# Optimization experiments

Hardware: AMD Instinct MI355X
Metric: run time of the kernel (lower is better)

Reference implementation:

```python
import jax, jax.numpy as jnp
import numpy as np

B, S, D = 8, 4096, 1024
EPS = 1e-8  # torch F.cosine_similarity default eps


def setup_inputs() -> dict:
    key = jax.random.key(0)
    kx, kwq, kbq, kwk, kbk = jax.random.split(key, 5)
    bound = 1.0 / np.sqrt(D)  # torch nn.Linear default init
    return {
        "x": jax.random.normal(kx, (B, S, D), dtype=jnp.float32),
        "Wq": jax.random.uniform(kwq, (D, D), jnp.float32, -bound, bound),
        "bq": jax.random.uniform(kbq, (D,), jnp.float32, -bound, bound),
        "Wk": jax.random.uniform(kwk, (D, D), jnp.float32, -bound, bound),
        "bk": jax.random.uniform(kbk, (D,), jnp.float32, -bound, bound),
    }


def reference(x, Wq, bq, Wk, bk):
    # ---- RoutingModule ----
    q = jnp.einsum("bsd,ed->bse", x, Wq) + bq                      # [B,S,D]
    x_roll = jnp.roll(x, shift=1, axis=1)                           # roll along seq
    k = jnp.einsum("bsd,ed->bse", x_roll, Wk) + bk                  # [B,S,D]
    qn = q / jnp.maximum(jnp.linalg.norm(q, axis=-1, keepdims=True), EPS)
    kn = k / jnp.maximum(jnp.linalg.norm(k, axis=-1, keepdims=True), EPS)
    cosine_sim = jnp.sum(qn * kn, axis=-1)                          # [B,S]
    p = 0.5 * (1.0 - cosine_sim)
    p = p.at[:, 0].set(1.0)
    b = (p >= 0.5).astype(x.dtype)                                  # [B,S]

    # ---- ragged compaction into padded buffer ----
    # Stable argsort moves selected positions to the front, preserving order.
    order = jnp.argsort(1.0 - b, axis=1)                            # [B,S] int
    gathered = jnp.take_along_axis(x, order[:, :, None], axis=1)    # [B,S,D]
    counts = jnp.sum(b, axis=1).astype(jnp.int32)                   # [B]
    valid = jnp.arange(S)[None, :] < counts[:, None]                # [B,S]
    # Padded to S (static max possible length) for jit-compatibility; torch
    # trims to the batch max, but all rows beyond each count are zeros here too.
    selected_padded = jnp.where(valid[:, :, None], gathered, 0.0)   # [B,S,D]
    return selected_padded, p, b
```

## Files before the change

kernel.cpp:

```cpp
#include <hip/hip_runtime.h>
#include <stdint.h>

#define Bb 8
#define Ss 4096
#define Dd 1024
#define Mm (Bb*Ss)
#define Kk 1024

typedef _Float16 half8 __attribute__((ext_vector_type(8)));
typedef _Float16 half4v __attribute__((ext_vector_type(4)));
typedef float f32x4 __attribute__((ext_vector_type(4)));

#define LO_SCALE 2048.0f
#define INV_LO_SCALE (1.0f/2048.0f)

__device__ __forceinline__ void gld_lds16(const void* g, void* l) {
  __builtin_amdgcn_global_load_lds(
      (const __attribute__((address_space(1))) unsigned int*)g,
      (__attribute__((address_space(3))) unsigned int*)l, 16, 0, 0);
}

__global__ void split_w3(const float* __restrict__ Gp, const float* __restrict__ Wq,
                         const float* __restrict__ Wk,
                         _Float16* __restrict__ Gh, _Float16* __restrict__ Gl,
                         _Float16* __restrict__ Wh) {
  const int which = blockIdx.y;
  const int i = blockIdx.x * 256 + threadIdx.x;
  float4 v;
  if (which == 0) {
    float4 v0 = ((const float4*)Gp)[i];
    float4 v1 = ((const float4*)(Gp + (size_t)Dd * Dd))[i];
    float4 v2 = ((const float4*)(Gp + (size_t)2 * Dd * Dd))[i];
    float4 v3 = ((const float4*)(Gp + (size_t)3 * Dd * Dd))[i];
    v.x = (v0.x + v1.x) + (v2.x + v3.x);
    v.y = (v0.y + v1.y) + (v2.y + v3.y);
    v.z = (v0.z + v1.z) + (v2.z + v3.z);
    v.w = (v0.w + v1.w) + (v2.w + v3.w);
  } else {
    const float* src = (which == 1) ? Wq : Wk;
    v = ((const float4*)src)[i];
  }
  _Float16 h0 = (_Float16)v.x, h1 = (_Float16)v.y, h2 = (_Float16)v.z, h3 = (_Float16)v.w;
  if (which == 0) {
    _Float16 l0 = (_Float16)((v.x - (float)h0) * LO_SCALE);
    _Float16 l1 = (_Float16)((v.y - (float)h1) * LO_SCALE);
    _Float16 l2 = (_Float16)((v.z - (float)h2) * LO_SCALE);
    _Float16 l3 = (_Float16)((v.w - (float)h3) * LO_SCALE);
    ((half4v*)Gh)[i] = (half4v){h0, h1, h2, h3};
    ((half4v*)Gl)[i] = (half4v){l0, l1, l2, l3};
  } else {
    _Float16* hi = (which == 1) ? Wh : Wh + (size_t)Dd * Dd;
    ((half4v*)hi)[i] = (half4v){h0, h1, h2, h3};
  }
}

__global__ void split_x(const float* __restrict__ X, const float* __restrict__ up,
                        const float* __restrict__ vp,
                        _Float16* __restrict__ Xh, _Float16* __restrict__ Xl,
                        float* __restrict__ a_u, float* __restrict__ a_v) {
  const int s = blockIdx.x * 4 + (threadIdx.x >> 6);
  const int lane = threadIdx.x & 63;
  float au = 0.f, av = 0.f;
#pragma unroll
  for (int c = 0; c < 4; ++c) {
    const int e = c * 256 + lane * 4;
    float4 xv = *(const float4*)&X[(size_t)s * Dd + e];
    float4 uv = {0.f, 0.f, 0.f, 0.f}, vv = {0.f, 0.f, 0.f, 0.f};
#pragma unroll
    for (int z = 0; z < 4; ++z) {
      float4 a = *(const float4*)&up[(size_t)z * Dd + e];
      float4 b = *(const float4*)&vp[(size_t)z * Dd + e];
      uv.x += a.x; uv.y += a.y; uv.z += a.z; uv.w += a.w;
      vv.x += b.x; vv.y += b.y; vv.z += b.z; vv.w += b.w;
    }
    _Float16 h0 = (_Float16)xv.x, h1 = (_Float16)xv.y, h2 = (_Float16)xv.z, h3 = (_Float16)xv.w;
    _Float16 l0 = (_Float16)((xv.x - (float)h0) * LO_SCALE);
    _Float16 l1 = (_Float16)((xv.y - (float)h1) * LO_SCALE);
    _Float16 l2 = (_Float16)((xv.z - (float)h2) * LO_SCALE);
    _Float16 l3 = (_Float16)((xv.w - (float)h3) * LO_SCALE);
    *(half4v*)&Xh[(size_t)s * Dd + e] = (half4v){h0, h1, h2, h3};
    *(half4v*)&Xl[(size_t)s * Dd + e] = (half4v){l0, l1, l2, l3};
    au += uv.x * xv.x + uv.y * xv.y + uv.z * xv.z + uv.w * xv.w;
    av += vv.x * xv.x + vv.y * xv.y + vv.z * xv.z + vv.w * xv.w;
  }
#pragma unroll
  for (int off = 32; off > 0; off >>= 1) {
    au += __shfl_xor(au, off);
    av += __shfl_xor(av, off);
  }
  if (lane == 0) { a_u[s] = au; a_v[s] = av; }
}

__global__ __launch_bounds__(256)
void gemm_g_part(const float* __restrict__ Wq, const float* __restrict__ Wk,
                 float* __restrict__ Gp) {
  __shared__ float As[16][64];
  __shared__ float Bs[16][64];
  const int t = threadIdx.x;
  const int m0 = blockIdx.y * 64, n0 = blockIdx.x * 64;
  const int kbase = blockIdx.z * 256;
  float acc[4][4];
#pragma unroll
  for (int a = 0; a < 4; ++a)
#pragma unroll
    for (int b = 0; b < 4; ++b) acc[a][b] = 0.f;
  for (int kc = 0; kc < 16; ++kc) {
    const int k0 = kbase + kc * 16;
#pragma unroll
    for (int l = 0; l < 4; ++l) {
      const int idx = l * 256 + t;
      const int kk = idx >> 6, mm = idx & 63;
      As[kk][mm] = Wq[(size_t)(k0 + kk) * Dd + m0 + mm];
      Bs[kk][mm] = Wk[(size_t)(k0 + kk) * Dd + n0 + mm];
    }
    __syncthreads();
    const int tm = (t & 15) * 4, tn = (t >> 4) * 4;
#pragma unroll
    for (int k = 0; k < 16; ++k) {
      float4 a4 = *(const float4*)&As[k][tm];
      float4 b4 = *(const float4*)&Bs[k][tn];
      const float aa[4] = {a4.x, a4.y, a4.z, a4.w};
      const float bb[4] = {b4.x, b4.y, b4.z, b4.w};
#pragma unroll
      for (int a = 0; a < 4; ++a)
#pragma unroll
        for (int b = 0; b < 4; ++b) acc[a][b] += aa[a] * bb[b];
    }
    __syncthreads();
  }
  float* dst = Gp + (size_t)blockIdx.z * Dd * Dd;
  const int tm = (t & 15) * 4, tn = (t >> 4) * 4;
#pragma unroll
  for (int a = 0; a < 4; ++a)
#pragma unroll
    for (int b = 0; b < 4; ++b)
      dst[(size_t)(m0 + tm + a) * Dd + n0 + tn + b] = acc[a][b];
}

__global__ void uvc_part(const float* __restrict__ Wq, const float* __restrict__ Wk,
                         const float* __restrict__ bq, const float* __restrict__ bk,
                         float* __restrict__ up, float* __restrict__ vp,
                         float* __restrict__ c) {
  const int bx = blockIdx.x;
  if (bx == 32) {
    const int lane = threadIdx.x;
    if (lane >= 64) return;
    float a = 0.f;
#pragma unroll
    for (int i = 0; i < 16; ++i) a += bq[lane * 16 + i] * bk[lane * 16 + i];
#pragma unroll
    for (int off = 32; off > 0; off >>= 1) a += __shfl_xor(a, off);
    if (lane == 0) *c = a;
    return;
  }
  const int echunk = bx & 3;
  const int which = (bx >> 2) & 1;
  const int dchunk = bx >> 3;
  const int d = dchunk * 256 + threadIdx.x;
  const float* W = which ? Wq : Wk;
  const float* bb = which ? bk : bq;
  float acc = 0.f;
  const int e0 = echunk * 256;
#pragma unroll 4
  for (int e = e0; e < e0 + 256; ++e) acc += bb[e] * W[(size_t)e * Dd + d];
  float* dst = which ? vp : up;
  dst[(size_t)echunk * Dd + d] = acc;
}

__global__ __launch_bounds__(256, 2)
void gemm_dot(const _Float16* __restrict__ Ah, const _Float16* __restrict__ Al,
              const _Float16* __restrict__ Gh, const _Float16* __restrict__ Gl,
              const float* __restrict__ X, float* __restrict__ pd) {
  __shared__ __align__(16) _Float16 smem[4 * 128 * 64];
  _Float16* AsH = smem;
  _Float16* AsL = smem + 8192;
  _Float16* BsH = smem + 16384;
  _Float16* BsL = smem + 24576;
  const int tid = threadIdx.x;
  const int wave = tid >> 6, lane = tid & 63;
  const int m0 = blockIdx.y * 128, n0 = blockIdx.x * 128;
  const int wm = (wave >> 1) * 64, wn = (wave & 1) * 64;
  const int fr = lane & 15, g = lane >> 4;
  const int srow8 = lane >> 3, s8 = lane & 7;

  f32x4 accH[4][4], accX[4][4];
#pragma unroll
  for (int i = 0; i < 4; ++i)
#pragma unroll
    for (int j = 0; j < 4; ++j) {
      accH[i][j] = (f32x4){0.f, 0.f, 0.f, 0.f};
      accX[i][j] = (f32x4){0.f, 0.f, 0.f, 0.f};
    }

  for (int kt = 0; kt < Kk / 64; ++kt) {
    const int k0 = kt * 64;
#pragma unroll
    for (int it = 0; it < 4; ++it) {
      const int R = wave * 32 + it * 8 + srow8;
      const int gcol = k0 + ((s8 ^ (R & 7)) * 8);
      const int ldsoff = (wave * 32 + it * 8) * 64;
      const size_t ga = (size_t)(m0 + R) * Kk + gcol;
      const size_t gb = (size_t)(n0 + R) * Kk + gcol;
      gld_lds16(Ah + ga, &AsH[ldsoff]);
      gld_lds16(Al + ga, &AsL[ldsoff]);
      gld_lds16(Gh + gb, &BsH[ldsoff]);
      gld_lds16(Gl + gb, &BsL[ldsoff]);
    }
    __syncthreads();
#pragma unroll
    for (int kk = 0; kk < 2; ++kk) {
      const int gg = kk * 4 + g;
      half8 bh[4], bl[4];
#pragma unroll
      for (int j = 0; j < 4; ++j) {
        const int R = wn + 16 * j + fr;
        const int sl = (gg ^ (R & 7)) * 8;
        bh[j] = *(const half8*)&BsH[R * 64 + sl];
        bl[j] = *(const half8*)&BsL[R * 64 + sl];
      }
#pragma unroll
      for (int i = 0; i < 4; ++i) {
        const int R = wm + 16 * i + fr;
        const int sl = (gg ^ (R & 7)) * 8;
        half8 ah = *(const half8*)&AsH[R * 64 + sl];
        half8 al = *(const half8*)&AsL[R * 64 + sl];
#pragma unroll
        for (int j = 0; j < 4; ++j) {
          accH[i][j] = __builtin_amdgcn_mfma_f32_16x16x32_f16(ah, bh[j], accH[i][j], 0, 0, 0);
          accX[i][j] = __builtin_amdgcn_mfma_f32_16x16x32_f16(ah, bl[j], accX[i][j], 0, 0, 0);
          accX[i][j] = __builtin_amdgcn_mfma_f32_16x16x32_f16(al, bh[j], accX[i][j], 0, 0, 0);
        }
      }
    }
    __syncthreads();
  }
  const int quad = lane >> 4;
  const int slot = blockIdx.x * 2 + (wave & 1);
#pragma unroll
  for (int i = 0; i < 4; ++i) {
#pragma unroll
    for (int r = 0; r < 4; ++r) {
      const int s = m0 + wm + 16 * i + quad * 4 + r;
      const int t = s + 1;
      float dsum = 0.f;
      if ((t & (Ss - 1)) != 0) {
        const float* xrow = X + (size_t)t * Dd + n0 + wn;
#pragma unroll
        for (int j = 0; j < 4; ++j) {
          float yv = accH[i][j][r] + accX[i][j][r] * INV_LO_SCALE;
          dsum += yv * xrow[16 * j + fr];
        }
      }
      dsum += __shfl_xor(dsum, 1);
      dsum += __shfl_xor(dsum, 2);
      dsum += __shfl_xor(dsum, 4);
      dsum += __shfl_xor(dsum, 8);
      if (fr == 0 && ((t & (Ss - 1)) != 0))
        pd[(size_t)slot * Mm + t] = dsum;
    }
  }
}

__global__ __launch_bounds__(256, 3)
void gemm_norm(const _Float16* __restrict__ Ah, const _Float16* __restrict__ Wh,
               const float* __restrict__ bq, const float* __restrict__ bk,
               float* __restrict__ pn) {
  __shared__ __align__(16) _Float16 smem[2 * 128 * 64];
  _Float16* NA = smem;
  _Float16* NB = smem + 8192;
  const int tid = threadIdx.x;
  const int wave = tid >> 6, lane = tid & 63;
  const int m0 = blockIdx.y * 128, n0 = blockIdx.x * 128;
  const int wm = (wave >> 1) * 64, wn = (wave & 1) * 64;
  const int fr = lane & 15, g = lane >> 4;
  const int srow8 = lane >> 3, s8 = lane & 7;

  f32x4 acc[4][4];
#pragma unroll
  for (int i = 0; i < 4; ++i)
#pragma unroll
    for (int j = 0; j < 4; ++j) acc[i][j] = (f32x4){0.f, 0.f, 0.f, 0.f};

  for (int kt = 0; kt < Kk / 64; ++kt) {
    const int k0 = kt * 64;
#pragma unroll
    for (int it = 0; it < 4; ++it) {
      const int R = wave * 32 + it * 8 + srow8;
      const int gcol = k0 + ((s8 ^ (R & 7)) * 8);
      const int ldsoff = (wave * 32 + it * 8) * 64;
      gld_lds16(Ah + (size_t)(m0 + R) * Kk + gcol, &NA[ldsoff]);
      gld_lds16(Wh + (size_t)(n0 + R) * Kk + gcol, &NB[ldsoff]);
    }
    __syncthreads();
#pragma unroll
    for (int kk = 0; kk < 2; ++kk) {
      const int gg = kk * 4 + g;
      half8 bh[4];
#pragma unroll
      for (int j = 0; j < 4; ++j) {
        const int R = wn + 16 * j + fr;
        bh[j] = *(const half8*)&NB[R * 64 + (gg ^ (R & 7)) * 8];
      }
#pragma unroll
      for (int i = 0; i < 4; ++i) {
        const int R = wm + 16 * i + fr;
        half8 ah = *(const half8*)&NA[R * 64 + (gg ^ (R & 7)) * 8];
#pragma unroll
        for (int j = 0; j < 4; ++j)
          acc[i][j] = __builtin_amdgcn_mfma_f32_16x16x32_f16(ah, bh[j], acc[i][j], 0, 0, 0);
      }
    }
    __syncthreads();
  }
  const int quad = lane >> 4;
  float bias_j[4];
#pragma unroll
  for (int j = 0; j < 4; ++j) {
    const int n = n0 + wn + 16 * j + fr;
    bias_j[j] = (n < Dd) ? bq[n] : bk[n - Dd];
  }
  const int slot = blockIdx.x * 2 + (wave & 1);
#pragma unroll
  for (int i = 0; i < 4; ++i) {
#pragma unroll
    for (int r = 0; r < 4; ++r) {
      float vsum = 0.f;
#pragma unroll
      for (int j = 0; j < 4; ++j) {
        float q = acc[i][j][r] + bias_j[j];
        vsum += q * q;
      }
      vsum += __shfl_xor(vsum, 1);
      vsum += __shfl_xor(vsum, 2);
      vsum += __shfl_xor(vsum, 4);
      vsum += __shfl_xor(vsum, 8);
      if (fr == 0)
        pn[(size_t)slot * Mm + (m0 + wm + 16 * i + quad * 4 + r)] = vsum;
    }
  }
}

__global__ void cos_final(const float* __restrict__ pd, const float* __restrict__ pn,
                          const float* __restrict__ a_u, const float* __restrict__ a_v,
                          const float* __restrict__ cptr,
                          float* __restrict__ p_out, float* __restrict__ b_out) {
  const int s = blockIdx.x * 256 + threadIdx.x;
  if ((s & (Ss - 1)) == 0) { p_out[s] = 1.0f; b_out[s] = 1.0f; return; }
  float dot = a_u[s - 1] + a_v[s] + *cptr;
#pragma unroll
  for (int sl = 0; sl < 16; ++sl) dot += pd[(size_t)sl * Mm + s];
  float nq = 0.f, nk = 0.f;
#pragma unroll
  for (int sl = 0; sl < 16; ++sl) nq += pn[(size_t)sl * Mm + s];
#pragma unroll
  for (int sl = 16; sl < 32; ++sl) nk += pn[(size_t)sl * Mm + (s - 1)];
  float denom = fmaxf(sqrtf(nq), 1e-8f) * fmaxf(sqrtf(nk), 1e-8f);
  float cs = dot / denom;
  float p = 0.5f * (1.0f - cs);
  p_out[s] = p;
  b_out[s] = (p >= 0.5f) ? 1.0f : 0.0f;
}

__global__ __launch_bounds__(1024)
void scan_flags(const float* __restrict__ b_out,
                int* __restrict__ sel, int* __restrict__ counts) {
  const int b = blockIdx.x;
  const int tid = threadIdx.x;
  const int lane = tid & 63;
  const int w = tid >> 6;
  __shared__ int wtot[16];
  float fv[4];
#pragma unroll
  for (int c = 0; c < 4; ++c) fv[c] = b_out[b * Ss + c * 1024 + tid];
  int running = 0;
#pragma unroll
  for (int c = 0; c < 4; ++c) {
    const bool f = fv[c] != 0.0f;
    unsigned long long m = __ballot(f);
    int pre = __popcll(m & ((1ull << lane) - 1ull));
    if (lane == 0) wtot[w] = __popcll(m);
    __syncthreads();
    int woff = 0, tot = 0;
#pragma unroll
    for (int ww = 0; ww < 16; ++ww) {
      int t = wtot[ww];
      if (ww < w) woff += t;
      tot += t;
    }
    if (f) sel[b * Ss + running + woff + pre] = c * 1024 + tid;
    running += tot;
    __syncthreads();
  }
  if (tid == 0) counts[b] = running;
}

__global__ void write_out(const float* __restrict__ x, const int* __restrict__ sel,
                          const int* __restrict__ counts, float* __restrict__ out) {
  const int blk = blockIdx.x;
  const int b = blk >> 12;
  const int r = blk & (Ss - 1);
  const int tid = threadIdx.x;
  float4 v = {0.f, 0.f, 0.f, 0.f};
  if (r < counts[b]) {
    const int src = sel[b * Ss + r];
    v = *(const float4*)&x[((size_t)b * Ss + src) * Dd + tid * 4];
  }
  *(float4*)&out[(size_t)blk * Dd + tid * 4] = v;
}

extern "C" void kernel_launch(void* const* d_in, const int* in_sizes, int n_in,
                              void* d_out, int out_size, void* d_ws, size_t ws_size,
                              hipStream_t stream) {
  const float* x  = (const float*)d_in[0];
  const float* Wq = (const float*)d_in[1];
  const float* bq = (const float*)d_in[2];
  const float* Wk = (const float*)d_in[3];
  const float* bk = (const float*)d_in[4];
  float* out = (float*)d_out;

  uint8_t* w = (uint8_t*)d_ws;
  _Float16* Xh = (_Float16*)w;   w += (size_t)Mm * Kk * 2;
  _Float16* Xl = (_Float16*)w;   w += (size_t)Mm * Kk * 2;
  float*    Gp = (float*)w;      w += (size_t)4 * Dd * Dd * 4;
  _Float16* Gh = (_Float16*)w;   w += (size_t)Dd * Dd * 2;
  _Float16* Gl = (_Float16*)w;   w += (size_t)Dd * Dd * 2;
  _Float16* Wh = (_Float16*)w;   w += (size_t)2 * Dd * Dd * 2;
  float* pd = (float*)w;         w += (size_t)16 * Mm * 4;
  float* pn = (float*)w;         w += (size_t)32 * Mm * 4;
  float* a_u = (float*)w;        w += (size_t)Mm * 4;
  float* a_v = (float*)w;        w += (size_t)Mm * 4;
  float* up  = (float*)w;        w += (size_t)4 * Dd * 4;
  float* vp  = (float*)w;        w += (size_t)4 * Dd * 4;
  float* cpt = (float*)w;        w += 64;
  int*   sel = (int*)w;          w += (size_t)Mm * 4;
  int*   counts = (int*)w;       w += 64;

  float* p_out = out + (size_t)Mm * Dd;
  float* b_out = p_out + Mm;

  gemm_g_part<<<dim3(16, 16, 4), 256, 0, stream>>>(Wq, Wk, Gp);
  uvc_part<<<33, 256, 0, stream>>>(Wq, Wk, bq, bk, up, vp, cpt);
  split_x<<<Mm / 4, 256, 0, stream>>>(x, up, vp, Xh, Xl, a_u, a_v);
  split_w3<<<dim3((Dd * Dd / 4) / 256, 3), 256, 0, stream>>>(Gp, Wq, Wk, Gh, Gl, Wh);
  gemm_norm<<<dim3(2 * Dd / 128, Mm / 128), 256, 0, stream>>>(Xh, Wh, bq, bk, pn);
  gemm_dot<<<dim3(Dd / 128, Mm / 128), 256, 0, stream>>>(Xh, Xl, Gh, Gl, x, pd);
  cos_final<<<Mm / 256, 256, 0, stream>>>(pd, pn, a_u, a_v, cpt, p_out, b_out);
  scan_flags<<<Bb, 1024, 0, stream>>>(b_out, sel, counts);
  write_out<<<Mm, 256, 0, stream>>>(x, sel, counts, out);
}
```

Baseline: 708.6 us.

## Interleave hi/lo halves and triple-buffer both GEMMs with larger tiles

The hi and lo fp16 splits of x and G are interleaved into one row-major buffer, so one async load brings both halves. Both GEMM kernels move to 512 threads with 256x128 tiles, a three-slot LDS ring with explicit vmcnt waits, a tile swizzle for locality, and raised wave priority around the MFMA blocks. Per-wave partial row sums are reduced in LDS before storing, which halves the partial-slot buffers that cos_final reads. The aim is to hide global-load latency and cut barriers and partial traffic, at the cost of more LDS use and register pressure.

```diff
diff --git a/kernel.cpp b/kernel.cpp
--- a/kernel.cpp
+++ b/kernel.cpp
@@ -22,8 +22,7 @@
 
 __global__ void split_w3(const float* __restrict__ Gp, const float* __restrict__ Wq,
                          const float* __restrict__ Wk,
-                         _Float16* __restrict__ Gh, _Float16* __restrict__ Gl,
-                         _Float16* __restrict__ Wh) {
+                         _Float16* __restrict__ G2, _Float16* __restrict__ Wh) {
   const int which = blockIdx.y;
   const int i = blockIdx.x * 256 + threadIdx.x;
   float4 v;
@@ -46,8 +45,9 @@
     _Float16 l1 = (_Float16)((v.y - (float)h1) * LO_SCALE);
     _Float16 l2 = (_Float16)((v.z - (float)h2) * LO_SCALE);
     _Float16 l3 = (_Float16)((v.w - (float)h3) * LO_SCALE);
-    ((half4v*)Gh)[i] = (half4v){h0, h1, h2, h3};
-    ((half4v*)Gl)[i] = (half4v){l0, l1, l2, l3};
+    const int n = i >> 8, c = i & 255;
+    ((half4v*)G2)[(size_t)n * 512 + c]       = (half4v){h0, h1, h2, h3};
+    ((half4v*)G2)[(size_t)n * 512 + 256 + c] = (half4v){l0, l1, l2, l3};
   } else {
     _Float16* hi = (which == 1) ? Wh : Wh + (size_t)Dd * Dd;
     ((half4v*)hi)[i] = (half4v){h0, h1, h2, h3};
@@ -56,7 +56,7 @@
 
 __global__ void split_x(const float* __restrict__ X, const float* __restrict__ up,
                         const float* __restrict__ vp,
-                        _Float16* __restrict__ Xh, _Float16* __restrict__ Xl,
+                        _Float16* __restrict__ X2,
                         float* __restrict__ a_u, float* __restrict__ a_v) {
   const int s = blockIdx.x * 4 + (threadIdx.x >> 6);
   const int lane = threadIdx.x & 63;
@@ -78,8 +78,8 @@
     _Float16 l1 = (_Float16)((xv.y - (float)h1) * LO_SCALE);
     _Float16 l2 = (_Float16)((xv.z - (float)h2) * LO_SCALE);
     _Float16 l3 = (_Float16)((xv.w - (float)h3) * LO_SCALE);
-    *(half4v*)&Xh[(size_t)s * Dd + e] = (half4v){h0, h1, h2, h3};
-    *(half4v*)&Xl[(size_t)s * Dd + e] = (half4v){l0, l1, l2, l3};
+    *(half4v*)&X2[(size_t)s * 2048 + e]        = (half4v){h0, h1, h2, h3};
+    *(half4v*)&X2[(size_t)s * 2048 + 1024 + e] = (half4v){l0, l1, l2, l3};
     au += uv.x * xv.x + uv.y * xv.y + uv.z * xv.z + uv.w * xv.w;
     av += vv.x * xv.x + vv.y * xv.y + vv.z * xv.z + vv.w * xv.w;
   }
@@ -167,86 +167,126 @@
   dst[(size_t)echunk * Dd + d] = acc;
 }
 
-__global__ __launch_bounds__(256, 2)
-void gemm_dot(const _Float16* __restrict__ Ah, const _Float16* __restrict__ Al,
-              const _Float16* __restrict__ Gh, const _Float16* __restrict__ Gl,
+
+__global__ __launch_bounds__(512, 2)
+void gemm_dot(const _Float16* __restrict__ X2, const _Float16* __restrict__ G2,
               const float* __restrict__ X, float* __restrict__ pd) {
-  __shared__ __align__(16) _Float16 smem[4 * 128 * 64];
-  _Float16* AsH = smem;
-  _Float16* AsL = smem + 8192;
-  _Float16* BsH = smem + 16384;
-  _Float16* BsL = smem + 24576;
+  __shared__ __align__(16) _Float16 smem[3 * 24576];
   const int tid = threadIdx.x;
   const int wave = tid >> 6, lane = tid & 63;
-  const int m0 = blockIdx.y * 128, n0 = blockIdx.x * 128;
-  const int wm = (wave >> 1) * 64, wn = (wave & 1) * 64;
-  const int fr = lane & 15, g = lane >> 4;
-  const int srow8 = lane >> 3, s8 = lane & 7;
-
-  f32x4 accH[4][4], accX[4][4];
-#pragma unroll
-  for (int i = 0; i < 4; ++i)
-#pragma unroll
-    for (int j = 0; j < 4; ++j) {
+  const int lin = blockIdx.y * 8 + blockIdx.x;
+  const int logical = (lin & 7) * 128 + (lin >> 3);
+  const int n0 = (logical & 7) * 128;
+  const int m0 = (logical >> 3) * 256;
+  const int wm = (wave >> 2) * 128;
+  const int wn = (wave & 3) * 32;
+  const int fr = lane & 15, g4 = lane >> 4;
+  const int sr = lane >> 3, sc = lane & 7;
+
+  size_t aoff[4];
+  size_t boff[2];
+#pragma unroll
+  for (int st = 0; st < 4; ++st) {
+    const int R = st * 64 + wave * 8 + sr;
+    const int u = sc ^ (R & 7);
+    aoff[st] = (size_t)(m0 + R) * 2048 + ((u & 3) << 3) + ((size_t)(u >> 2) << 10);
+  }
+#pragma unroll
+  for (int st = 0; st < 2; ++st) {
+    const int R = st * 64 + wave * 8 + sr;
+    const int u = sc ^ (R & 7);
+    boff[st] = (size_t)(n0 + R) * 2048 + ((u & 3) << 3) + ((size_t)(u >> 2) << 10);
+  }
+  int aro[2][8], bro[2][2];
+#pragma unroll
+  for (int i = 0; i < 8; ++i) {
+    const int Ra = wm + i * 16 + fr;
+    aro[0][i] = Ra * 64 + ((g4 ^ (Ra & 7)) << 3);
+    aro[1][i] = Ra * 64 + (((4 | g4) ^ (Ra & 7)) << 3);
+  }
+#pragma unroll
+  for (int j = 0; j < 2; ++j) {
+    const int Rb = wn + j * 16 + fr;
+    bro[0][j] = Rb * 64 + ((g4 ^ (Rb & 7)) << 3);
+    bro[1][j] = Rb * 64 + (((4 | g4) ^ (Rb & 7)) << 3);
+  }
+
+  f32x4 accH[8][2], accX[8][2];
+#pragma unroll
+  for (int i = 0; i < 8; ++i)
+#pragma unroll
+    for (int j = 0; j < 2; ++j) {
       accH[i][j] = (f32x4){0.f, 0.f, 0.f, 0.f};
       accX[i][j] = (f32x4){0.f, 0.f, 0.f, 0.f};
     }
 
-  for (int kt = 0; kt < Kk / 64; ++kt) {
-    const int k0 = kt * 64;
-#pragma unroll
-    for (int it = 0; it < 4; ++it) {
-      const int R = wave * 32 + it * 8 + srow8;
-      const int gcol = k0 + ((s8 ^ (R & 7)) * 8);
-      const int ldsoff = (wave * 32 + it * 8) * 64;
-      const size_t ga = (size_t)(m0 + R) * Kk + gcol;
-      const size_t gb = (size_t)(n0 + R) * Kk + gcol;
-      gld_lds16(Ah + ga, &AsH[ldsoff]);
-      gld_lds16(Al + ga, &AsL[ldsoff]);
-      gld_lds16(Gh + gb, &BsH[ldsoff]);
-      gld_lds16(Gl + gb, &BsL[ldsoff]);
-    }
-    __syncthreads();
-#pragma unroll
-    for (int kk = 0; kk < 2; ++kk) {
-      const int gg = kk * 4 + g;
-      half8 bh[4], bl[4];
-#pragma unroll
-      for (int j = 0; j < 4; ++j) {
-        const int R = wn + 16 * j + fr;
-        const int sl = (gg ^ (R & 7)) * 8;
-        bh[j] = *(const half8*)&BsH[R * 64 + sl];
-        bl[j] = *(const half8*)&BsL[R * 64 + sl];
+#define DOT_STAGE(kt, slot) do {                                      \
+    const size_t kof = (size_t)(kt) * 32;                             \
+    _Float16* sb_ = smem + (slot) * 24576;                            \
+    gld_lds16(X2 + aoff[0] + kof, sb_ + 0 * 4096 + wave * 512);       \
+    gld_lds16(X2 + aoff[1] + kof, sb_ + 1 * 4096 + wave * 512);       \
+    gld_lds16(X2 + aoff[2] + kof, sb_ + 2 * 4096 + wave * 512);       \
+    gld_lds16(X2 + aoff[3] + kof, sb_ + 3 * 4096 + wave * 512);       \
+    gld_lds16(G2 + boff[0] + kof, sb_ + 16384 + 0 * 4096 + wave * 512); \
+    gld_lds16(G2 + boff[1] + kof, sb_ + 16384 + 1 * 4096 + wave * 512); \
+  } while (0)
+
+  DOT_STAGE(0, 0);
+  DOT_STAGE(1, 1);
+  int slot = 0;
+  for (int kt = 0; kt < 32; ++kt) {
+    if (kt < 31) asm volatile("s_waitcnt vmcnt(6)" ::: "memory");
+    else         asm volatile("s_waitcnt vmcnt(0)" ::: "memory");
+    __builtin_amdgcn_s_barrier();
+    asm volatile("" ::: "memory");
+    if (kt + 2 < 32) {
+      int s2 = slot + 2; if (s2 >= 3) s2 -= 3;
+      DOT_STAGE(kt + 2, s2);
+    }
+    const _Float16* A  = smem + slot * 24576;
+    const _Float16* Bm = A + 16384;
+    half8 bh[2], bl[2];
+#pragma unroll
+    for (int j = 0; j < 2; ++j) {
+      bh[j] = *(const half8*)&Bm[bro[0][j]];
+      bl[j] = *(const half8*)&Bm[bro[1][j]];
+    }
+#pragma unroll
+    for (int ph = 0; ph < 4; ++ph) {
+      const int i0 = ph * 2;
+      half8 ah0 = *(const half8*)&A[aro[0][i0]];
+      half8 al0 = *(const half8*)&A[aro[1][i0]];
+      half8 ah1 = *(const half8*)&A[aro[0][i0 + 1]];
+      half8 al1 = *(const half8*)&A[aro[1][i0 + 1]];
+      __builtin_amdgcn_s_setprio(1);
+#pragma unroll
+      for (int j = 0; j < 2; ++j) {
+        accH[i0][j]     = __builtin_amdgcn_mfma_f32_16x16x32_f16(ah0, bh[j], accH[i0][j], 0, 0, 0);
+        accX[i0][j]     = __builtin_amdgcn_mfma_f32_16x16x32_f16(ah0, bl[j], accX[i0][j], 0, 0, 0);
+        accX[i0][j]     = __builtin_amdgcn_mfma_f32_16x16x32_f16(al0, bh[j], accX[i0][j], 0, 0, 0);
+        accH[i0 + 1][j] = __builtin_amdgcn_mfma_f32_16x16x32_f16(ah1, bh[j], accH[i0 + 1][j], 0, 0, 0);
+        accX[i0 + 1][j] = __builtin_amdgcn_mfma_f32_16x16x32_f16(ah1, bl[j], accX[i0 + 1][j], 0, 0, 0);
+        accX[i0 + 1][j] = __builtin_amdgcn_mfma_f32_16x16x32_f16(al1, bh[j], accX[i0 + 1][j], 0, 0, 0);
       }
-#pragma unroll
-      for (int i = 0; i < 4; ++i) {
-        const int R = wm + 16 * i + fr;
-        const int sl = (gg ^ (R & 7)) * 8;
-        half8 ah = *(const half8*)&AsH[R * 64 + sl];
-        half8 al = *(const half8*)&AsL[R * 64 + sl];
-#pragma unroll
-        for (int j = 0; j < 4; ++j) {
-          accH[i][j] = __builtin_amdgcn_mfma_f32_16x16x32_f16(ah, bh[j], accH[i][j], 0, 0, 0);
-          accX[i][j] = __builtin_amdgcn_mfma_f32_16x16x32_f16(ah, bl[j], accX[i][j], 0, 0, 0);
-          accX[i][j] = __builtin_amdgcn_mfma_f32_16x16x32_f16(al, bh[j], accX[i][j], 0, 0, 0);
-        }
-      }
-    }
-    __syncthreads();
-  }
-  const int quad = lane >> 4;
-  const int slot = blockIdx.x * 2 + (wave & 1);
-#pragma unroll
-  for (int i = 0; i < 4; ++i) {
+      __builtin_amdgcn_s_setprio(0);
+    }
+    __builtin_amdgcn_sched_barrier(0);
+    slot = (slot == 2) ? 0 : slot + 1;
+  }
+
+  float* scratch = (float*)smem;
+  const int quad = g4;
+#pragma unroll
+  for (int i = 0; i < 8; ++i) {
 #pragma unroll
     for (int r = 0; r < 4; ++r) {
-      const int s = m0 + wm + 16 * i + quad * 4 + r;
-      const int t = s + 1;
+      const int row = wm + 16 * i + quad * 4 + r;
+      const int t = m0 + row + 1;
       float dsum = 0.f;
       if ((t & (Ss - 1)) != 0) {
         const float* xrow = X + (size_t)t * Dd + n0 + wn;
 #pragma unroll
-        for (int j = 0; j < 4; ++j) {
+        for (int j = 0; j < 2; ++j) {
           float yv = accH[i][j][r] + accX[i][j][r] * INV_LO_SCALE;
           dsum += yv * xrow[16 * j + fr];
         }
@@ -255,78 +295,138 @@
       dsum += __shfl_xor(dsum, 2);
       dsum += __shfl_xor(dsum, 4);
       dsum += __shfl_xor(dsum, 8);
-      if (fr == 0 && ((t & (Ss - 1)) != 0))
-        pd[(size_t)slot * Mm + t] = dsum;
-    }
-  }
-}
-
-__global__ __launch_bounds__(256, 3)
-void gemm_norm(const _Float16* __restrict__ Ah, const _Float16* __restrict__ Wh,
+      if (fr == 0) scratch[row * 4 + (wave & 3)] = dsum;
+    }
+  }
+  __syncthreads();
+  if (tid < 256) {
+    const int t = m0 + tid + 1;
+    if ((t & (Ss - 1)) != 0) {
+      float v = scratch[tid * 4] + scratch[tid * 4 + 1] +
+                scratch[tid * 4 + 2] + scratch[tid * 4 + 3];
+      pd[(size_t)(logical & 7) * Mm + t] = v;
+    }
+  }
+}
+
+__global__ __launch_bounds__(512, 2)
+void gemm_norm(const _Float16* __restrict__ X2, const _Float16* __restrict__ Wh,
                const float* __restrict__ bq, const float* __restrict__ bk,
                float* __restrict__ pn) {
-  __shared__ __align__(16) _Float16 smem[2 * 128 * 64];
-  _Float16* NA = smem;
-  _Float16* NB = smem + 8192;
+  __shared__ __align__(16) _Float16 smem[3 * 24576];
   const int tid = threadIdx.x;
   const int wave = tid >> 6, lane = tid & 63;
-  const int m0 = blockIdx.y * 128, n0 = blockIdx.x * 128;
-  const int wm = (wave >> 1) * 64, wn = (wave & 1) * 64;
-  const int fr = lane & 15, g = lane >> 4;
-  const int srow8 = lane >> 3, s8 = lane & 7;
-
-  f32x4 acc[4][4];
-#pragma unroll
-  for (int i = 0; i < 4; ++i)
-#pragma unroll
-    for (int j = 0; j < 4; ++j) acc[i][j] = (f32x4){0.f, 0.f, 0.f, 0.f};
-
-  for (int kt = 0; kt < Kk / 64; ++kt) {
-    const int k0 = kt * 64;
-#pragma unroll
-    for (int it = 0; it < 4; ++it) {
-      const int R = wave * 32 + it * 8 + srow8;
-      const int gcol = k0 + ((s8 ^ (R & 7)) * 8);
-      const int ldsoff = (wave * 32 + it * 8) * 64;
-      gld_lds16(Ah + (size_t)(m0 + R) * Kk + gcol, &NA[ldsoff]);
-      gld_lds16(Wh + (size_t)(n0 + R) * Kk + gcol, &NB[ldsoff]);
-    }
-    __syncthreads();
-#pragma unroll
-    for (int kk = 0; kk < 2; ++kk) {
-      const int gg = kk * 4 + g;
-      half8 bh[4];
-#pragma unroll
-      for (int j = 0; j < 4; ++j) {
-        const int R = wn + 16 * j + fr;
-        bh[j] = *(const half8*)&NB[R * 64 + (gg ^ (R & 7)) * 8];
+  const int lin = blockIdx.y * 16 + blockIdx.x;
+  const int logical = (lin & 7) * 256 + (lin >> 3);
+  const int n0 = (logical & 15) * 128;
+  const int m0 = (logical >> 4) * 256;
+  const int wm = (wave >> 2) * 128;
+  const int wn = (wave & 3) * 32;
+  const int fr = lane & 15, g4 = lane >> 4;
+  const int sr = lane >> 3, sc = lane & 7;
+
+  size_t aoff[4];
+  size_t boff[2];
+#pragma unroll
+  for (int st = 0; st < 4; ++st) {
+    const int R = st * 64 + wave * 8 + sr;
+    const int u = sc ^ (R & 7);
+    aoff[st] = (size_t)(m0 + R) * 2048 + ((size_t)u << 3);
+  }
+#pragma unroll
+  for (int st = 0; st < 2; ++st) {
+    const int R = st * 64 + wave * 8 + sr;
+    const int u = sc ^ (R & 7);
+    boff[st] = (size_t)(n0 + R) * 1024 + ((size_t)u << 3);
+  }
+  int aro[2][8], bro[2][2];
+#pragma unroll
+  for (int i = 0; i < 8; ++i) {
+    const int Ra = wm + i * 16 + fr;
+    aro[0][i] = Ra * 64 + ((g4 ^ (Ra & 7)) << 3);
+    aro[1][i] = Ra * 64 + (((4 | g4) ^ (Ra & 7)) << 3);
+  }
+#pragma unroll
+  for (int j = 0; j < 2; ++j) {
+    const int Rb = wn + j * 16 + fr;
+    bro[0][j] = Rb * 64 + ((g4 ^ (Rb & 7)) << 3);
+    bro[1][j] = Rb * 64 + (((4 | g4) ^ (Rb & 7)) << 3);
+  }
+
+  f32x4 acc[8][2];
+#pragma unroll
+  for (int i = 0; i < 8; ++i)
+#pragma unroll
+    for (int j = 0; j < 2; ++j) acc[i][j] = (f32x4){0.f, 0.f, 0.f, 0.f};
+
+#define NRM_STAGE(kt, slot) do {                                      \
+    const size_t kof = (size_t)(kt) * 64;                             \
+    _Float16* sb_ = smem + (slot) * 24576;                            \
+    gld_lds16(X2 + aoff[0] + kof, sb_ + 0 * 4096 + wave * 512);       \
+    gld_lds16(X2 + aoff[1] + kof, sb_ + 1 * 4096 + wave * 512);       \
+    gld_lds16(X2 + aoff[2] + kof, sb_ + 2 * 4096 + wave * 512);       \
+    gld_lds16(X2 + aoff[3] + kof, sb_ + 3 * 4096 + wave * 512);       \
+    gld_lds16(Wh + boff[0] + kof, sb_ + 16384 + 0 * 4096 + wave * 512); \
+    gld_lds16(Wh + boff[1] + kof, sb_ + 16384 + 1 * 4096 + wave * 512); \
+  } while (0)
+
+  NRM_STAGE(0, 0);
+  NRM_STAGE(1, 1);
+  int slot = 0;
+  for (int kt = 0; kt < 16; ++kt) {
+    if (kt < 15) asm volatile("s_waitcnt vmcnt(6)" ::: "memory");
+    else         asm volatile("s_waitcnt vmcnt(0)" ::: "memory");
+    __builtin_amdgcn_s_barrier();
+    asm volatile("" ::: "memory");
+    if (kt + 2 < 16) {
+      int s2 = slot + 2; if (s2 >= 3) s2 -= 3;
+      NRM_STAGE(kt + 2, s2);
+    }
+    const _Float16* A  = smem + slot * 24576;
+    const _Float16* Bm = A + 16384;
+    half8 b0[2], b1[2];
+#pragma unroll
+    for (int j = 0; j < 2; ++j) {
+      b0[j] = *(const half8*)&Bm[bro[0][j]];
+      b1[j] = *(const half8*)&Bm[bro[1][j]];
+    }
+#pragma unroll
+    for (int ph = 0; ph < 4; ++ph) {
+      const int i0 = ph * 2;
+      half8 a00 = *(const half8*)&A[aro[0][i0]];
+      half8 a01 = *(const half8*)&A[aro[1][i0]];
+      half8 a10 = *(const half8*)&A[aro[0][i0 + 1]];
+      half8 a11 = *(const half8*)&A[aro[1][i0 + 1]];
+      __builtin_amdgcn_s_setprio(1);
+#pragma unroll
+      for (int j = 0; j < 2; ++j) {
+        acc[i0][j]     = __builtin_amdgcn_mfma_f32_16x16x32_f16(a00, b0[j], acc[i0][j], 0, 0, 0);
+        acc[i0][j]     = __builtin_amdgcn_mfma_f32_16x16x32_f16(a01, b1[j], acc[i0][j], 0, 0, 0);
+        acc[i0 + 1][j] = __builtin_amdgcn_mfma_f32_16x16x32_f16(a10, b0[j], acc[i0 + 1][j], 0, 0, 0);
+        acc[i0 + 1][j] = __builtin_amdgcn_mfma_f32_16x16x32_f16(a11, b1[j], acc[i0 + 1][j], 0, 0, 0);
       }
-#pragma unroll
-      for (int i = 0; i < 4; ++i) {
-        const int R = wm + 16 * i + fr;
-        half8 ah = *(const half8*)&NA[R * 64 + (gg ^ (R & 7)) * 8];
-#pragma unroll
-        for (int j = 0; j < 4; ++j)
-          acc[i][j] = __builtin_amdgcn_mfma_f32_16x16x32_f16(ah, bh[j], acc[i][j], 0, 0, 0);
-      }
-    }
-    __syncthreads();
-  }
-  const int quad = lane >> 4;
-  float bias_j[4];
-#pragma unroll
-  for (int j = 0; j < 4; ++j) {
+      __builtin_amdgcn_s_setprio(0);
+    }
+    __builtin_amdgcn_sched_barrier(0);
+    slot = (slot == 2) ? 0 : slot + 1;
+  }
+
+  float bias_j[2];
+#pragma unroll
+  for (int j = 0; j < 2; ++j) {
     const int n = n0 + wn + 16 * j + fr;
     bias_j[j] = (n < Dd) ? bq[n] : bk[n - Dd];
   }
-  const int slot = blockIdx.x * 2 + (wave & 1);
-#pragma unroll
-  for (int i = 0; i < 4; ++i) {
+  float* scratch = (float*)smem;
+  const int quad = g4;
+#pragma unroll
+  for (int i = 0; i < 8; ++i) {
 #pragma unroll
     for (int r = 0; r < 4; ++r) {
+      const int row = wm + 16 * i + quad * 4 + r;
       float vsum = 0.f;
 #pragma unroll
-      for (int j = 0; j < 4; ++j) {
+      for (int j = 0; j < 2; ++j) {
         float q = acc[i][j][r] + bias_j[j];
         vsum += q * q;
       }
@@ -334,9 +434,14 @@
       vsum += __shfl_xor(vsum, 2);
       vsum += __shfl_xor(vsum, 4);
       vsum += __shfl_xor(vsum, 8);
-      if (fr == 0)
-        pn[(size_t)slot * Mm + (m0 + wm + 16 * i + quad * 4 + r)] = vsum;
-    }
+      if (fr == 0) scratch[row * 4 + (wave & 3)] = vsum;
+    }
+  }
+  __syncthreads();
+  if (tid < 256) {
+    float v = scratch[tid * 4] + scratch[tid * 4 + 1] +
+              scratch[tid * 4 + 2] + scratch[tid * 4 + 3];
+    pn[(size_t)(logical & 15) * Mm + (m0 + tid)] = v;
   }
 }
 
@@ -348,12 +453,12 @@
   if ((s & (Ss - 1)) == 0) { p_out[s] = 1.0f; b_out[s] = 1.0f; return; }
   float dot = a_u[s - 1] + a_v[s] + *cptr;
 #pragma unroll
-  for (int sl = 0; sl < 16; ++sl) dot += pd[(size_t)sl * Mm + s];
+  for (int sl = 0; sl < 8; ++sl) dot += pd[(size_t)sl * Mm + s];
   float nq = 0.f, nk = 0.f;
 #pragma unroll
-  for (int sl = 0; sl < 16; ++sl) nq += pn[(size_t)sl * Mm + s];
-#pragma unroll
-  for (int sl = 16; sl < 32; ++sl) nk += pn[(size_t)sl * Mm + (s - 1)];
+  for (int sl = 0; sl < 8; ++sl) nq += pn[(size_t)sl * Mm + s];
+#pragma unroll
+  for (int sl = 8; sl < 16; ++sl) nk += pn[(size_t)sl * Mm + (s - 1)];
   float denom = fmaxf(sqrtf(nq), 1e-8f) * fmaxf(sqrtf(nk), 1e-8f);
   float cs = dot / denom;
   float p = 0.5f * (1.0f - cs);
@@ -419,31 +524,29 @@
   float* out = (float*)d_out;
 
   uint8_t* w = (uint8_t*)d_ws;
-  _Float16* Xh = (_Float16*)w;   w += (size_t)Mm * Kk * 2;
-  _Float16* Xl = (_Float16*)w;   w += (size_t)Mm * Kk * 2;
-  float*    Gp = (float*)w;      w += (size_t)4 * Dd * Dd * 4;
-  _Float16* Gh = (_Float16*)w;   w += (size_t)Dd * Dd * 2;
-  _Float16* Gl = (_Float16*)w;   w += (size_t)Dd * Dd * 2;
-  _Float16* Wh = (_Float16*)w;   w += (size_t)2 * Dd * Dd * 2;
-  float* pd = (float*)w;         w += (size_t)16 * Mm * 4;
-  float* pn = (float*)w;         w += (size_t)32 * Mm * 4;
-  float* a_u = (float*)w;        w += (size_t)Mm * 4;
-  float* a_v = (float*)w;        w += (size_t)Mm * 4;
-  float* up  = (float*)w;        w += (size_t)4 * Dd * 4;
-  float* vp  = (float*)w;        w += (size_t)4 * Dd * 4;
-  float* cpt = (float*)w;        w += 64;
-  int*   sel = (int*)w;          w += (size_t)Mm * 4;
-  int*   counts = (int*)w;       w += 64;
+  _Float16* X2 = (_Float16*)w; w += (size_t)Mm * 2048 * 2;
+  float*    Gp = (float*)w;    w += (size_t)4 * Dd * Dd * 4;
+  _Float16* G2 = (_Float16*)w; w += (size_t)Dd * 2048 * 2;
+  _Float16* Wh = (_Float16*)w; w += (size_t)2 * Dd * Dd * 2;
+  float* pd = (float*)w;       w += (size_t)8 * Mm * 4;
+  float* pn = (float*)w;       w += (size_t)16 * Mm * 4;
+  float* a_u = (float*)w;      w += (size_t)Mm * 4;
+  float* a_v = (float*)w;      w += (size_t)Mm * 4;
+  float* up  = (float*)w;      w += (size_t)4 * Dd * 4;
+  float* vp  = (float*)w;      w += (size_t)4 * Dd * 4;
+  float* cpt = (float*)w;      w += 64;
+  int*   sel = (int*)w;        w += (size_t)Mm * 4;
+  int*   counts = (int*)w;     w += 64;
 
   float* p_out = out + (size_t)Mm * Dd;
   float* b_out = p_out + Mm;
 
   gemm_g_part<<<dim3(16, 16, 4), 256, 0, stream>>>(Wq, Wk, Gp);
   uvc_part<<<33, 256, 0, stream>>>(Wq, Wk, bq, bk, up, vp, cpt);
-  split_x<<<Mm / 4, 256, 0, stream>>>(x, up, vp, Xh, Xl, a_u, a_v);
-  split_w3<<<dim3((Dd * Dd / 4) / 256, 3), 256, 0, stream>>>(Gp, Wq, Wk, Gh, Gl, Wh);
-  gemm_norm<<<dim3(2 * Dd / 128, Mm / 128), 256, 0, stream>>>(Xh, Wh, bq, bk, pn);
-  gemm_dot<<<dim3(Dd / 128, Mm / 128), 256, 0, stream>>>(Xh, Xl, Gh, Gl, x, pd);
+  split_x<<<Mm / 4, 256, 0, stream>>>(x, up, vp, X2, a_u, a_v);
+  split_w3<<<dim3((Dd * Dd / 4) / 256, 3), 256, 0, stream>>>(Gp, Wq, Wk, G2, Wh);
+  gemm_norm<<<dim3(16, Mm / 256), 512, 0, stream>>>(X2, Wh, bq, bk, pn);
+  gemm_dot<<<dim3(8, Mm / 256), 512, 0, stream>>>(X2, G2, x, pd);
   cos_final<<<Mm / 256, 256, 0, stream>>>(pd, pn, a_u, a_v, cpt, p_out, b_out);
   scan_flags<<<Bb, 1024, 0, stream>>>(b_out, sel, counts);
   write_out<<<Mm, 256, 0, stream>>>(x, sel, counts, out);
```

New measurement: 782.1 us. 1.1x slower.

## Interleave hi/lo fp16 splits and read G operand directly from global memory

Applied to the files above, without the earlier changes.

Computes G = Wq^T Wk in one non-split-K kernel that writes hi/lo fp16 halves directly, which removes the partial-sum buffer and the reduction in the split kernel. X and G hi/lo halves are interleaved per row into single buffers. gemm_dot no longer stages the G tile in LDS: B fragments are loaded straight from global or L2, which halves shared memory use and may raise occupancy. The cost is uncoalesced, uncached-in-LDS B reads repeated across waves, and gemm_g now runs with only 256 blocks and a long K loop.

```diff
diff --git a/kernel.cpp b/kernel.cpp
--- a/kernel.cpp
+++ b/kernel.cpp
@@ -20,43 +20,74 @@
       (__attribute__((address_space(3))) unsigned int*)l, 16, 0, 0);
 }
 
-__global__ void split_w3(const float* __restrict__ Gp, const float* __restrict__ Wq,
-                         const float* __restrict__ Wk,
-                         _Float16* __restrict__ Gh, _Float16* __restrict__ Gl,
+#define MFMA16(d, a, b) d = __builtin_amdgcn_mfma_f32_16x16x32_f16(a, b, d, 0, 0, 0)
+
+__global__ __launch_bounds__(256)
+void gemm_g(const float* __restrict__ Wq, const float* __restrict__ Wk,
+            _Float16* __restrict__ G2) {
+  __shared__ float As[16][64];
+  __shared__ float Bs[16][64];
+  const int t = threadIdx.x;
+  const int m0 = blockIdx.y * 64, n0 = blockIdx.x * 64;
+  float acc[4][4];
+#pragma unroll
+  for (int a = 0; a < 4; ++a)
+#pragma unroll
+    for (int b = 0; b < 4; ++b) acc[a][b] = 0.f;
+  for (int kc = 0; kc < 64; ++kc) {
+    const int k0 = kc * 16;
+#pragma unroll
+    for (int l = 0; l < 4; ++l) {
+      const int idx = l * 256 + t;
+      const int kk = idx >> 6, mm = idx & 63;
+      As[kk][mm] = Wq[(size_t)(k0 + kk) * Dd + m0 + mm];
+      Bs[kk][mm] = Wk[(size_t)(k0 + kk) * Dd + n0 + mm];
+    }
+    __syncthreads();
+    const int tm = (t & 15) * 4, tn = (t >> 4) * 4;
+#pragma unroll
+    for (int k = 0; k < 16; ++k) {
+      float4 a4 = *(const float4*)&As[k][tm];
+      float4 b4 = *(const float4*)&Bs[k][tn];
+      const float aa[4] = {a4.x, a4.y, a4.z, a4.w};
+      const float bb[4] = {b4.x, b4.y, b4.z, b4.w};
+#pragma unroll
+      for (int a = 0; a < 4; ++a)
+#pragma unroll
+        for (int b = 0; b < 4; ++b) acc[a][b] += aa[a] * bb[b];
+    }
+    __syncthreads();
+  }
+  const int tm = (t & 15) * 4, tn = (t >> 4) * 4;
+#pragma unroll
+  for (int a = 0; a < 4; ++a) {
+    half4v hv, lv;
+#pragma unroll
+    for (int b = 0; b < 4; ++b) {
+      float v = acc[a][b];
+      _Float16 h = (_Float16)v;
+      hv[b] = h;
+      lv[b] = (_Float16)((v - (float)h) * LO_SCALE);
+    }
+    const size_t row = (size_t)(m0 + tm + a) * 2048;
+    *(half4v*)&G2[row + n0 + tn] = hv;
+    *(half4v*)&G2[row + 1024 + n0 + tn] = lv;
+  }
+}
+
+__global__ void split_w2(const float* __restrict__ Wq, const float* __restrict__ Wk,
                          _Float16* __restrict__ Wh) {
   const int which = blockIdx.y;
   const int i = blockIdx.x * 256 + threadIdx.x;
-  float4 v;
-  if (which == 0) {
-    float4 v0 = ((const float4*)Gp)[i];
-    float4 v1 = ((const float4*)(Gp + (size_t)Dd * Dd))[i];
-    float4 v2 = ((const float4*)(Gp + (size_t)2 * Dd * Dd))[i];
-    float4 v3 = ((const float4*)(Gp + (size_t)3 * Dd * Dd))[i];
-    v.x = (v0.x + v1.x) + (v2.x + v3.x);
-    v.y = (v0.y + v1.y) + (v2.y + v3.y);
-    v.z = (v0.z + v1.z) + (v2.z + v3.z);
-    v.w = (v0.w + v1.w) + (v2.w + v3.w);
-  } else {
-    const float* src = (which == 1) ? Wq : Wk;
-    v = ((const float4*)src)[i];
-  }
-  _Float16 h0 = (_Float16)v.x, h1 = (_Float16)v.y, h2 = (_Float16)v.z, h3 = (_Float16)v.w;
-  if (which == 0) {
-    _Float16 l0 = (_Float16)((v.x - (float)h0) * LO_SCALE);
-    _Float16 l1 = (_Float16)((v.y - (float)h1) * LO_SCALE);
-    _Float16 l2 = (_Float16)((v.z - (float)h2) * LO_SCALE);
-    _Float16 l3 = (_Float16)((v.w - (float)h3) * LO_SCALE);
-    ((half4v*)Gh)[i] = (half4v){h0, h1, h2, h3};
-    ((half4v*)Gl)[i] = (half4v){l0, l1, l2, l3};
-  } else {
-    _Float16* hi = (which == 1) ? Wh : Wh + (size_t)Dd * Dd;
-    ((half4v*)hi)[i] = (half4v){h0, h1, h2, h3};
-  }
+  const float* src = which ? Wk : Wq;
+  float4 v = ((const float4*)src)[i];
+  _Float16* dst = Wh + (size_t)which * Dd * Dd;
+  ((half4v*)dst)[i] = (half4v){(_Float16)v.x, (_Float16)v.y, (_Float16)v.z, (_Float16)v.w};
 }
 
 __global__ void split_x(const float* __restrict__ X, const float* __restrict__ up,
                         const float* __restrict__ vp,
-                        _Float16* __restrict__ Xh, _Float16* __restrict__ Xl,
+                        _Float16* __restrict__ X2,
                         float* __restrict__ a_u, float* __restrict__ a_v) {
   const int s = blockIdx.x * 4 + (threadIdx.x >> 6);
   const int lane = threadIdx.x & 63;
@@ -78,8 +109,8 @@
     _Float16 l1 = (_Float16)((xv.y - (float)h1) * LO_SCALE);
     _Float16 l2 = (_Float16)((xv.z - (float)h2) * LO_SCALE);
     _Float16 l3 = (_Float16)((xv.w - (float)h3) * LO_SCALE);
-    *(half4v*)&Xh[(size_t)s * Dd + e] = (half4v){h0, h1, h2, h3};
-    *(half4v*)&Xl[(size_t)s * Dd + e] = (half4v){l0, l1, l2, l3};
+    *(half4v*)&X2[(size_t)s * 2048 + e]        = (half4v){h0, h1, h2, h3};
+    *(half4v*)&X2[(size_t)s * 2048 + 1024 + e] = (half4v){l0, l1, l2, l3};
     au += uv.x * xv.x + uv.y * xv.y + uv.z * xv.z + uv.w * xv.w;
     av += vv.x * xv.x + vv.y * xv.y + vv.z * xv.z + vv.w * xv.w;
   }
@@ -89,52 +120,6 @@
     av += __shfl_xor(av, off);
   }
   if (lane == 0) { a_u[s] = au; a_v[s] = av; }
-}
-
-__global__ __launch_bounds__(256)
-void gemm_g_part(const float* __restrict__ Wq, const float* __restrict__ Wk,
-                 float* __restrict__ Gp) {
-  __shared__ float As[16][64];
-  __shared__ float Bs[16][64];
-  const int t = threadIdx.x;
-  const int m0 = blockIdx.y * 64, n0 = blockIdx.x * 64;
-  const int kbase = blockIdx.z * 256;
-  float acc[4][4];
-#pragma unroll
-  for (int a = 0; a < 4; ++a)
-#pragma unroll
-    for (int b = 0; b < 4; ++b) acc[a][b] = 0.f;
-  for (int kc = 0; kc < 16; ++kc) {
-    const int k0 = kbase + kc * 16;
-#pragma unroll
-    for (int l = 0; l < 4; ++l) {
-      const int idx = l * 256 + t;
-      const int kk = idx >> 6, mm = idx & 63;
-      As[kk][mm] = Wq[(size_t)(k0 + kk) * Dd + m0 + mm];
-      Bs[kk][mm] = Wk[(size_t)(k0 + kk) * Dd + n0 + mm];
-    }
-    __syncthreads();
-    const int tm = (t & 15) * 4, tn = (t >> 4) * 4;
-#pragma unroll
-    for (int k = 0; k < 16; ++k) {
-      float4 a4 = *(const float4*)&As[k][tm];
-      float4 b4 = *(const float4*)&Bs[k][tn];
-      const float aa[4] = {a4.x, a4.y, a4.z, a4.w};
-      const float bb[4] = {b4.x, b4.y, b4.z, b4.w};
-#pragma unroll
-      for (int a = 0; a < 4; ++a)
-#pragma unroll
-        for (int b = 0; b < 4; ++b) acc[a][b] += aa[a] * bb[b];
-    }
-    __syncthreads();
-  }
-  float* dst = Gp + (size_t)blockIdx.z * Dd * Dd;
-  const int tm = (t & 15) * 4, tn = (t >> 4) * 4;
-#pragma unroll
-  for (int a = 0; a < 4; ++a)
-#pragma unroll
-    for (int b = 0; b < 4; ++b)
-      dst[(size_t)(m0 + tm + a) * Dd + n0 + tn + b] = acc[a][b];
 }
 
 __global__ void uvc_part(const float* __restrict__ Wq, const float* __restrict__ Wk,
@@ -168,14 +153,11 @@
 }
 
 __global__ __launch_bounds__(256, 2)
-void gemm_dot(const _Float16* __restrict__ Ah, const _Float16* __restrict__ Al,
-              const _Float16* __restrict__ Gh, const _Float16* __restrict__ Gl,
+void gemm_dot(const _Float16* __restrict__ X2, const _Float16* __restrict__ G2,
               const float* __restrict__ X, float* __restrict__ pd) {
-  __shared__ __align__(16) _Float16 smem[4 * 128 * 64];
+  __shared__ __align__(16) _Float16 smem[2 * 128 * 64];
   _Float16* AsH = smem;
   _Float16* AsL = smem + 8192;
-  _Float16* BsH = smem + 16384;
-  _Float16* BsL = smem + 24576;
   const int tid = threadIdx.x;
   const int wave = tid >> 6, lane = tid & 63;
   const int m0 = blockIdx.y * 128, n0 = blockIdx.x * 128;
@@ -192,6 +174,11 @@
       accX[i][j] = (f32x4){0.f, 0.f, 0.f, 0.f};
     }
 
+  const _Float16* brow[4];
+#pragma unroll
+  for (int j = 0; j < 4; ++j)
+    brow[j] = G2 + (size_t)(n0 + wn + 16 * j + fr) * 2048;
+
   for (int kt = 0; kt < Kk / 64; ++kt) {
     const int k0 = kt * 64;
 #pragma unroll
@@ -199,12 +186,9 @@
       const int R = wave * 32 + it * 8 + srow8;
       const int gcol = k0 + ((s8 ^ (R & 7)) * 8);
       const int ldsoff = (wave * 32 + it * 8) * 64;
-      const size_t ga = (size_t)(m0 + R) * Kk + gcol;
-      const size_t gb = (size_t)(n0 + R) * Kk + gcol;
-      gld_lds16(Ah + ga, &AsH[ldsoff]);
-      gld_lds16(Al + ga, &AsL[ldsoff]);
-      gld_lds16(Gh + gb, &BsH[ldsoff]);
-      gld_lds16(Gl + gb, &BsL[ldsoff]);
+      const size_t ga = (size_t)(m0 + R) * 2048 + gcol;
+      gld_lds16(X2 + ga, &AsH[ldsoff]);
+      gld_lds16(X2 + ga + 1024, &AsL[ldsoff]);
     }
     __syncthreads();
 #pragma unroll
@@ -213,10 +197,9 @@
       half8 bh[4], bl[4];
 #pragma unroll
       for (int j = 0; j < 4; ++j) {
-        const int R = wn + 16 * j + fr;
-        const int sl = (gg ^ (R & 7)) * 8;
-        bh[j] = *(const half8*)&BsH[R * 64 + sl];
-        bl[j] = *(const half8*)&BsL[R * 64 + sl];
+        const _Float16* bp = brow[j] + k0 + gg * 8;
+        bh[j] = *(const half8*)bp;
+        bl[j] = *(const half8*)(bp + 1024);
       }
 #pragma unroll
       for (int i = 0; i < 4; ++i) {
@@ -226,9 +209,9 @@
         half8 al = *(const half8*)&AsL[R * 64 + sl];
 #pragma unroll
         for (int j = 0; j < 4; ++j) {
-          accH[i][j] = __builtin_amdgcn_mfma_f32_16x16x32_f16(ah, bh[j], accH[i][j], 0, 0, 0);
-          accX[i][j] = __builtin_amdgcn_mfma_f32_16x16x32_f16(ah, bl[j], accX[i][j], 0, 0, 0);
-          accX[i][j] = __builtin_amdgcn_mfma_f32_16x16x32_f16(al, bh[j], accX[i][j], 0, 0, 0);
+          MFMA16(accH[i][j], ah, bh[j]);
+          MFMA16(accX[i][j], ah, bl[j]);
+          MFMA16(accX[i][j], al, bh[j]);
         }
       }
     }
@@ -262,7 +245,7 @@
 }
 
 __global__ __launch_bounds__(256, 3)
-void gemm_norm(const _Float16* __restrict__ Ah, const _Float16* __restrict__ Wh,
+void gemm_norm(const _Float16* __restrict__ X2, const _Float16* __restrict__ Wh,
                const float* __restrict__ bq, const float* __restrict__ bk,
                float* __restrict__ pn) {
   __shared__ __align__(16) _Float16 smem[2 * 128 * 64];
@@ -288,7 +271,7 @@
       const int R = wave * 32 + it * 8 + srow8;
       const int gcol = k0 + ((s8 ^ (R & 7)) * 8);
       const int ldsoff = (wave * 32 + it * 8) * 64;
-      gld_lds16(Ah + (size_t)(m0 + R) * Kk + gcol, &NA[ldsoff]);
+      gld_lds16(X2 + (size_t)(m0 + R) * 2048 + gcol, &NA[ldsoff]);
       gld_lds16(Wh + (size_t)(n0 + R) * Kk + gcol, &NB[ldsoff]);
     }
     __syncthreads();
@@ -307,7 +290,7 @@
         half8 ah = *(const half8*)&NA[R * 64 + (gg ^ (R & 7)) * 8];
 #pragma unroll
         for (int j = 0; j < 4; ++j)
-          acc[i][j] = __builtin_amdgcn_mfma_f32_16x16x32_f16(ah, bh[j], acc[i][j], 0, 0, 0);
+          MFMA16(acc[i][j], ah, bh[j]);
       }
     }
     __syncthreads();
@@ -419,31 +402,28 @@
   float* out = (float*)d_out;
 
   uint8_t* w = (uint8_t*)d_ws;
-  _Float16* Xh = (_Float16*)w;   w += (size_t)Mm * Kk * 2;
-  _Float16* Xl = (_Float16*)w;   w += (size_t)Mm * Kk * 2;
-  float*    Gp = (float*)w;      w += (size_t)4 * Dd * Dd * 4;
-  _Float16* Gh = (_Float16*)w;   w += (size_t)Dd * Dd * 2;
-  _Float16* Gl = (_Float16*)w;   w += (size_t)Dd * Dd * 2;
-  _Float16* Wh = (_Float16*)w;   w += (size_t)2 * Dd * Dd * 2;
-  float* pd = (float*)w;         w += (size_t)16 * Mm * 4;
-  float* pn = (float*)w;         w += (size_t)32 * Mm * 4;
-  float* a_u = (float*)w;        w += (size_t)Mm * 4;
-  float* a_v = (float*)w;        w += (size_t)Mm * 4;
-  float* up  = (float*)w;        w += (size_t)4 * Dd * 4;
-  float* vp  = (float*)w;        w += (size_t)4 * Dd * 4;
-  float* cpt = (float*)w;        w += 64;
-  int*   sel = (int*)w;          w += (size_t)Mm * 4;
-  int*   counts = (int*)w;       w += 64;
+  _Float16* X2 = (_Float16*)w; w += (size_t)Mm * 2048 * 2;
+  _Float16* G2 = (_Float16*)w; w += (size_t)Dd * 2048 * 2;
+  _Float16* Wh = (_Float16*)w; w += (size_t)2 * Dd * Dd * 2;
+  float* pd = (float*)w;       w += (size_t)16 * Mm * 4;
+  float* pn = (float*)w;       w += (size_t)32 * Mm * 4;
+  float* a_u = (float*)w;      w += (size_t)Mm * 4;
+  float* a_v = (float*)w;      w += (size_t)Mm * 4;
+  float* up  = (float*)w;      w += (size_t)4 * Dd * 4;
+  float* vp  = (float*)w;      w += (size_t)4 * Dd * 4;
+  float* cpt = (float*)w;      w += 64;
+  int*   sel = (int*)w;        w += (size_t)Mm * 4;
+  int*   counts = (int*)w;     w += 64;
 
   float* p_out = out + (size_t)Mm * Dd;
   float* b_out = p_out + Mm;
 
-  gemm_g_part<<<dim3(16, 16, 4), 256, 0, stream>>>(Wq, Wk, Gp);
+  gemm_g<<<dim3(16, 16), 256, 0, stream>>>(Wq, Wk, G2);
   uvc_part<<<33, 256, 0, stream>>>(Wq, Wk, bq, bk, up, vp, cpt);
-  split_x<<<Mm / 4, 256, 0, stream>>>(x, up, vp, Xh, Xl, a_u, a_v);
-  split_w3<<<dim3((Dd * Dd / 4) / 256, 3), 256, 0, stream>>>(Gp, Wq, Wk, Gh, Gl, Wh);
-  gemm_norm<<<dim3(2 * Dd / 128, Mm / 128), 256, 0, stream>>>(Xh, Wh, bq, bk, pn);
-  gemm_dot<<<dim3(Dd / 128, Mm / 128), 256, 0, stream>>>(Xh, Xl, Gh, Gl, x, pd);
+  split_w2<<<dim3(1024, 2), 256, 0, stream>>>(Wq, Wk, Wh);
+  split_x<<<Mm / 4, 256, 0, stream>>>(x, up, vp, X2, a_u, a_v);
+  gemm_norm<<<dim3(2 * Dd / 128, Mm / 128), 256, 0, stream>>>(X2, Wh, bq, bk, pn);
+  gemm_dot<<<dim3(Dd / 128, Mm / 128), 256, 0, stream>>>(X2, G2, x, pd);
   cos_final<<<Mm / 256, 256, 0, stream>>>(pd, pn, a_u, a_v, cpt, p_out, b_out);
   scan_flags<<<Bb, 1024, 0, stream>>>(b_out, sel, counts);
   write_out<<<Mm, 256, 0, stream>>>(x, sel, counts, out);
```

After: 902.4 us. 27.4% more time.
